# Optimization experiments

Measured on AMD Instinct MI355X. Metric: run time of the kernel, lower is better.

Reference implementation:

```python
import jax, jax.numpy as jnp
import numpy as np

PI = np.pi
WIN = (8, 8)
N = WIN[0] * WIN[1]          # 64 tokens per window
NUM_HEADS = 8
DIM = 256
HEAD_DIM = DIM // NUM_HEADS  # 32
P = 4                        # Fourier series order (hardcoded in module)
W_RES = 64                   # input_resolution[1]
SCALE = HEAD_DIM ** -0.5
B_ = 1024                    # num_windows * batch


def _azimuth():
    # relative_coords[:, :, 1] from the torch module: relative column offsets
    ch = np.arange(WIN[0])
    cw = np.arange(WIN[1])
    gh, gw = np.meshgrid(ch, cw, indexing='ij')
    cf = np.stack([gh.ravel(), gw.ravel()])          # (2, N)
    rel = cf[:, :, None] - cf[:, None, :]            # (2, N, N)
    return jnp.asarray(rel[1], dtype=jnp.float32)    # (N, N)


def setup_inputs() -> dict:
    key = jax.random.key(0)
    ks = jax.random.split(key, 12)
    std = 0.02
    return {
        'x': jax.random.normal(ks[0], (B_, N, DIM), dtype=jnp.float32),
        'D': jax.random.uniform(ks[1], (B_, N), dtype=jnp.float32),
        'a_p': std * jax.random.normal(ks[2], (P + 1, NUM_HEADS), dtype=jnp.float32),
        'b_p': std * jax.random.normal(ks[3], (P, NUM_HEADS), dtype=jnp.float32),
        'a_r': std * jax.random.normal(ks[4], (P + 1, NUM_HEADS), dtype=jnp.float32),
        'b_r': std * jax.random.normal(ks[5], (P, NUM_HEADS), dtype=jnp.float32),
        'qkv_w': std * jax.random.normal(ks[6], (3 * DIM, DIM), dtype=jnp.float32),
        'qkv_b': jnp.zeros((3 * DIM,), dtype=jnp.float32),
        'proj_w': std * jax.random.normal(ks[7], (DIM, DIM), dtype=jnp.float32),
        'proj_b': jnp.zeros((DIM,), dtype=jnp.float32),
    }


def reference(x, D, a_p, b_p, a_r, b_r, qkv_w, qkv_b, proj_w, proj_b):
    B, n, C = x.shape

    # ---- azimuth Fourier bias: A_phi, shape (H, N, N) ----
    az = _azimuth() * (2.0 * PI / W_RES)                       # (N, N)
    ii = jnp.arange(1, P + 1, dtype=x.dtype)[:, None, None]    # (P, 1, 1)
    cosP = jnp.cos(ii * az)                                    # (P, N, N)
    sinP = jnp.sin(ii * az)
    A_phi = (jnp.einsum('ph,pij->hij', a_p[1:], cosP)
             + jnp.einsum('ph,pij->hij', b_p, sinP)) / P + a_p[0][:, None, None]

    # ---- radius Fourier bias: A_r, shape (B, N, N, H); rad[b,i,j] = D[b,j] - D[b,i] ----
    rad = D[:, None, :] - D[:, :, None]                        # (B, N, N)
    r_max = 2.0                                                # module overwrites r_max = 2
    A_r = jnp.zeros(rad.shape + (NUM_HEADS,), dtype=x.dtype)
    for i in range(1, P + 1):
        arg = rad * (2.0 * PI * i / r_max)
        A_r = A_r + jnp.cos(arg)[..., None] * a_r[i] + jnp.sin(arg)[..., None] * b_r[i - 1]
    A_r = A_r / P + a_r[0]                                     # (B, N, N, H)

    # ---- attention ----
    qkv = (x @ qkv_w.T + qkv_b).reshape(B, n, 3, NUM_HEADS, HEAD_DIM)
    qkv = qkv.transpose(2, 0, 3, 1, 4)                         # (3, B, H, N, hd)
    q, k, v = qkv[0], qkv[1], qkv[2]
    attn = jnp.einsum('bhid,bhjd->bhij', q * SCALE, k)
    attn = attn + A_phi[None] + A_r.transpose(0, 3, 1, 2)
    attn = jax.nn.softmax(attn, axis=-1)
    out = jnp.einsum('bhij,bhjd->bhid', attn, v)
    out = out.transpose(0, 2, 1, 3).reshape(B, n, C)
    return out @ proj_w.T + proj_b
```

## Files before the change

kernel.cpp:

```cpp
#include <hip/hip_runtime.h>
#include <hip/hip_bf16.h>


using short8  = __attribute__((ext_vector_type(8))) short;
using short4v = __attribute__((ext_vector_type(4))) short;
using floatx4 = __attribute__((ext_vector_type(4))) float;
using uint4v  = __attribute__((ext_vector_type(4))) unsigned int;

#define PI_F    3.14159265358979323846f
#define SCALE_F 0.17677669529663687f

__device__ __forceinline__ short bfs(float x) {
  __hip_bfloat16 h = __float2bfloat16(x);
  return __builtin_bit_cast(short, h);
}

__device__ __forceinline__ unsigned pk2(float a, float b) {
  unsigned lo = (unsigned short)bfs(a);
  unsigned hi = (unsigned short)bfs(b);
  return lo | (hi << 16);
}

__global__ void prep_kernel(const float* __restrict__ qw,
                            const float* __restrict__ pw,
                            __hip_bfloat16* __restrict__ dst) {
  int g = blockIdx.x * 256 + threadIdx.x;
  const float4* src;
  __hip_bfloat16* d;
  if (g < 49152) { src = (const float4*)qw + g; d = dst + g * 4; }
  else { int g2 = g - 49152; src = (const float4*)pw + g2; d = dst + 196608 + g2 * 4; }
  float4 v = *src;
  d[0] = __float2bfloat16(v.x);
  d[1] = __float2bfloat16(v.y);
  d[2] = __float2bfloat16(v.z);
  d[3] = __float2bfloat16(v.w);
}

__device__ __forceinline__ void fourier_feats(float dv, int col, float* f) {
  float s1, c1; __sincosf(PI_F * dv, &s1, &c1);
  float c2 = c1*c1 - s1*s1, s2 = 2.f*s1*c1;
  float c3 = c2*c1 - s2*s1, s3 = s2*c1 + c2*s1;
  float c4 = c2*c2 - s2*s2, s4 = 2.f*s2*c2;
  float sa1, ca1; __sincosf((2.f * PI_F / 64.f) * (float)col, &sa1, &ca1);
  float ca2 = ca1*ca1 - sa1*sa1, sa2 = 2.f*sa1*ca1;
  float ca3 = ca2*ca1 - sa2*sa1, sa3 = sa2*ca1 + ca2*sa1;
  float ca4 = ca2*ca2 - sa2*sa2, sa4 = 2.f*sa2*ca2;
  f[0]=c1;  f[1]=c2;  f[2]=c3;  f[3]=c4;
  f[4]=s1;  f[5]=s2;  f[6]=s3;  f[7]=s4;
  f[8]=ca1; f[9]=ca2; f[10]=ca3; f[11]=ca4;
  f[12]=sa1; f[13]=sa2; f[14]=sa3; f[15]=sa4;
}

__global__ __launch_bounds__(256) void win_kernel(
    const float* __restrict__ x, const float* __restrict__ D,
    const float* __restrict__ a_p, const float* __restrict__ b_p,
    const float* __restrict__ a_r, const float* __restrict__ b_r,
    const __hip_bfloat16* __restrict__ wq, const float* __restrict__ qkv_b,
    const __hip_bfloat16* __restrict__ pwb, const float* __restrict__ pb,
    float* __restrict__ out)
{
  __shared__ __align__(16) __hip_bfloat16 sX  [64 * 256];
  __shared__ __align__(16) __hip_bfloat16 sStr[4 * 4096];
  __shared__ __align__(16) __hip_bfloat16 sQf [64 * 32];

  const int tid = threadIdx.x;
  const int lane = tid & 63, w = tid >> 6;
  const int laneN = lane & 15, laneQ = lane >> 4;
  const int b = blockIdx.x;
  const floatx4 fzero = {0.f, 0.f, 0.f, 0.f};
  const short8 zero8 = {0, 0, 0, 0, 0, 0, 0, 0};

  char* xb = (char*)sX;
  char* sb = (char*)sStr + w * 8192;

  float f[16];
  fourier_feats(D[b * 64 + lane], lane & 7, f);

  const float4* xg = (const float4*)(x + (size_t)b * 16384);
  #pragma unroll 4
  for (int it = 0; it < 16; ++it) {
    int g = tid + it * 256;
    float4 v = xg[g];
    int t = g >> 6;
    int off = (t * 512 + (g & 63) * 8) ^ ((t & 7) << 4);
    short4v pk = { bfs(v.x), bfs(v.y), bfs(v.z), bfs(v.w) };
    *(short4v*)(xb + off) = pk;
  }
  if (tid < 64) {
    int t = tid;
    uint4v q0 = { pk2(f[0],f[1]),  pk2(f[2],f[3]),  pk2(f[4],f[5]),   pk2(f[6],f[7]) };
    uint4v q1 = { pk2(f[8],f[9]),  pk2(f[10],f[11]),pk2(f[12],f[13]), pk2(f[14],f[15]) };
    uint4v zz = { 0u, 0u, 0u, 0u };
    char* qb = (char*)sQf;
    *(uint4v*)(qb + ((t * 64 +  0) ^ ((t & 3) << 4))) = q0;
    *(uint4v*)(qb + ((t * 64 + 16) ^ ((t & 3) << 4))) = q1;
    *(uint4v*)(qb + ((t * 64 + 32) ^ ((t & 3) << 4))) = zz;
    *(uint4v*)(qb + ((t * 64 + 48) ^ ((t & 3) << 4))) = zz;
  }
  __syncthreads();

  for (int hi = 0; hi < 2; ++hi) {
    const int hh = w + hi * 4;

    const __hip_bfloat16* wqQ = wq + (size_t)(      hh*32 + laneN) * 256 + laneQ * 8;
    const __hip_bfloat16* wqK = wq + (size_t)(256 + hh*32 + laneN) * 256 + laneQ * 8;
    const __hip_bfloat16* wqV = wq + (size_t)(512 + hh*32 + laneN) * 256 + laneQ * 8;

    short8 qf[4];
    {
      floatx4 Qa[4][2];
      #pragma unroll
      for (int mt = 0; mt < 4; ++mt) { Qa[mt][0]=fzero; Qa[mt][1]=fzero; }
      __builtin_amdgcn_s_setprio(1);
      #pragma unroll
      for (int kk = 0; kk < 8; ++kk) {
        short8 a4[4];
        #pragma unroll
        for (int mt = 0; mt < 4; ++mt) {
          int off = ((mt*16 + laneN) * 512 + kk*64 + laneQ*16) ^ ((laneN & 7) << 4);
          a4[mt] = *(const short8*)(xb + off);
        }
        #pragma unroll
        for (int ont = 0; ont < 2; ++ont) {
          short8 fq = *(const short8*)(wqQ + (size_t)ont*16*256 + kk*32);
          #pragma unroll
          for (int mt = 0; mt < 4; ++mt)
            Qa[mt][ont] = __builtin_amdgcn_mfma_f32_16x16x32_bf16(fq, a4[mt], Qa[mt][ont], 0, 0, 0);
        }
      }
      __builtin_amdgcn_s_setprio(0);
      float4 b0 = *(const float4*)&qkv_b[hh*32 +      laneQ*4];
      float4 b1 = *(const float4*)&qkv_b[hh*32 + 16 + laneQ*4];
      float qba[2][4] = {{b0.x,b0.y,b0.z,b0.w},{b1.x,b1.y,b1.z,b1.w}};
      #pragma unroll
      for (int mt = 0; mt < 4; ++mt)
        #pragma unroll
        for (int ont = 0; ont < 2; ++ont) {
          short4v pq;
          #pragma unroll
          for (int r = 0; r < 4; ++r)
            pq[r] = bfs((Qa[mt][ont][r] + qba[ont][r]) * SCALE_F);
          int off = ((mt*16 + laneN) * 64 + ont*32 + laneQ*8) ^ ((laneN & 3) << 4);
          *(short4v*)(sb + off) = pq;
        }
      #pragma unroll
      for (int ct = 0; ct < 4; ++ct)
        qf[ct] = *(const short8*)(sb + (((ct*16 + laneN) * 64 + laneQ*16) ^ ((laneN & 3) << 4)));
    }

    short8 kf[4];
    {
      floatx4 Ka[4][2];
      #pragma unroll
      for (int mt = 0; mt < 4; ++mt) { Ka[mt][0]=fzero; Ka[mt][1]=fzero; }
      __builtin_amdgcn_s_setprio(1);
      #pragma unroll
      for (int kk = 0; kk < 8; ++kk) {
        short8 a4[4];
        #pragma unroll
        for (int mt = 0; mt < 4; ++mt) {
          int off = ((mt*16 + laneN) * 512 + kk*64 + laneQ*16) ^ ((laneN & 7) << 4);
          a4[mt] = *(const short8*)(xb + off);
        }
        #pragma unroll
        for (int ont = 0; ont < 2; ++ont) {
          short8 fk = *(const short8*)(wqK + (size_t)ont*16*256 + kk*32);
          #pragma unroll
          for (int mt = 0; mt < 4; ++mt)
            Ka[mt][ont] = __builtin_amdgcn_mfma_f32_16x16x32_bf16(fk, a4[mt], Ka[mt][ont], 0, 0, 0);
        }
      }
      __builtin_amdgcn_s_setprio(0);
      float4 b0 = *(const float4*)&qkv_b[256 + hh*32 +      laneQ*4];
      float4 b1 = *(const float4*)&qkv_b[256 + hh*32 + 16 + laneQ*4];
      float kba[2][4] = {{b0.x,b0.y,b0.z,b0.w},{b1.x,b1.y,b1.z,b1.w}};
      #pragma unroll
      for (int mt = 0; mt < 4; ++mt)
        #pragma unroll
        for (int ont = 0; ont < 2; ++ont) {
          short4v pk;
          #pragma unroll
          for (int r = 0; r < 4; ++r)
            pk[r] = bfs(Ka[mt][ont][r] + kba[ont][r]);
          int off = ((mt*16 + laneN) * 64 + ont*32 + laneQ*8) ^ ((laneN & 3) << 4);
          *(short4v*)(sb + off) = pk;
        }
      #pragma unroll
      for (int rt = 0; rt < 4; ++rt)
        kf[rt] = *(const short8*)(sb + (((rt*16 + laneN) * 64 + laneQ*16) ^ ((laneN & 3) << 4)));
    }

    short8 kmf[4];
    {
      float m0[4], m1[4], m2[4], m3[4];
      #pragma unroll
      for (int p = 0; p < 4; ++p) {
        float ar = a_r[(p+1)*8 + hh], br = b_r[p*8 + hh];
        float ap = a_p[(p+1)*8 + hh], bp = b_p[p*8 + hh];
        m0[p] = (ar*f[p]     + br*f[4+p])  * 0.25f;
        m1[p] = (ar*f[4+p]   - br*f[p])    * 0.25f;
        m2[p] = (ap*f[8+p]   - bp*f[12+p]) * 0.25f;
        m3[p] = (ap*f[12+p]  + bp*f[8+p])  * 0.25f;
      }
      uint4v k0 = { pk2(m0[0],m0[1]), pk2(m0[2],m0[3]), pk2(m1[0],m1[1]), pk2(m1[2],m1[3]) };
      uint4v k1 = { pk2(m2[0],m2[1]), pk2(m2[2],m2[3]), pk2(m3[0],m3[1]), pk2(m3[2],m3[3]) };
      *(uint4v*)(sb + lane * 32)      = k0;
      *(uint4v*)(sb + lane * 32 + 16) = k1;
      #pragma unroll
      for (int rt = 0; rt < 4; ++rt) {
        short8 t8 = *(const short8*)(sb + (rt*16 + laneN) * 32 + (laneQ & 1) * 16);
        kmf[rt] = (laneQ < 2) ? t8 : zero8;
      }
    }
    short8 qff[4];
    #pragma unroll
    for (int ct = 0; ct < 4; ++ct)
      qff[ct] = *(const short8*)((char*)sQf + (((ct*16 + laneN) * 64 + laneQ*16) ^ ((laneN & 3) << 4)));

    short8 vf[2][2];
    {
      floatx4 Va[4][2];
      #pragma unroll
      for (int mt = 0; mt < 4; ++mt) { Va[mt][0]=fzero; Va[mt][1]=fzero; }
      __builtin_amdgcn_s_setprio(1);
      #pragma unroll
      for (int kk = 0; kk < 8; ++kk) {
        short8 a4[4];
        #pragma unroll
        for (int mt = 0; mt < 4; ++mt) {
          int off = ((mt*16 + laneN) * 512 + kk*64 + laneQ*16) ^ ((laneN & 7) << 4);
          a4[mt] = *(const short8*)(xb + off);
        }
        #pragma unroll
        for (int ont = 0; ont < 2; ++ont) {
          short8 fv = *(const short8*)(wqV + (size_t)ont*16*256 + kk*32);
          #pragma unroll
          for (int mt = 0; mt < 4; ++mt)
            Va[mt][ont] = __builtin_amdgcn_mfma_f32_16x16x32_bf16(a4[mt], fv, Va[mt][ont], 0, 0, 0);
        }
      }
      __builtin_amdgcn_s_setprio(0);
      float bv0 = qkv_b[512 + hh*32 +      laneN];
      float bv1 = qkv_b[512 + hh*32 + 16 + laneN];
      #pragma unroll
      for (int mt = 0; mt < 4; ++mt)
        #pragma unroll
        for (int ont = 0; ont < 2; ++ont) {
          float bv = ont ? bv1 : bv0;
          short4v pv;
          #pragma unroll
          for (int r = 0; r < 4; ++r)
            pv[r] = bfs(Va[mt][ont][r] + bv);
          int off = ((ont*16 + laneN) * 128 + mt*32 + laneQ*8) ^ ((laneN & 7) << 4);
          *(short4v*)(sb + off) = pv;
        }
      #pragma unroll
      for (int ont = 0; ont < 2; ++ont)
        #pragma unroll
        for (int kb = 0; kb < 2; ++kb)
          vf[ont][kb] = *(const short8*)(sb + (((ont*16 + laneN) * 128 + kb*64 + laneQ*16) ^ ((laneN & 7) << 4)));
    }

    floatx4 Oa[2][4];
    #pragma unroll
    for (int cp = 0; cp < 2; ++cp) {
      floatx4 S[4][2];
      __builtin_amdgcn_s_setprio(1);
      #pragma unroll
      for (int rt = 0; rt < 4; ++rt)
        #pragma unroll
        for (int cc = 0; cc < 2; ++cc) {
          int ct = cp * 2 + cc;
          S[rt][cc] = __builtin_amdgcn_mfma_f32_16x16x32_bf16(kf[rt], qf[ct], fzero, 0, 0, 0);
          S[rt][cc] = __builtin_amdgcn_mfma_f32_16x16x32_bf16(kmf[rt], qff[ct], S[rt][cc], 0, 0, 0);
        }
      __builtin_amdgcn_s_setprio(0);

      float inv2[2];
      #pragma unroll
      for (int cc = 0; cc < 2; ++cc) {
        float mx = S[0][cc][0];
        #pragma unroll
        for (int rt = 0; rt < 4; ++rt)
          #pragma unroll
          for (int r = 0; r < 4; ++r)
            mx = fmaxf(mx, S[rt][cc][r]);
        mx = fmaxf(mx, __shfl_xor(mx, 16));
        mx = fmaxf(mx, __shfl_xor(mx, 32));
        float sum = 0.f;
        #pragma unroll
        for (int rt = 0; rt < 4; ++rt)
          #pragma unroll
          for (int r = 0; r < 4; ++r) {
            S[rt][cc][r] = __expf(S[rt][cc][r] - mx);
            sum += S[rt][cc][r];
          }
        sum += __shfl_xor(sum, 16);
        sum += __shfl_xor(sum, 32);
        inv2[cc] = __builtin_amdgcn_rcpf(sum);
      }

      #pragma unroll
      for (int cc = 0; cc < 2; ++cc)
        #pragma unroll
        for (int rt = 0; rt < 4; ++rt) {
          short4v pp;
          #pragma unroll
          for (int r = 0; r < 4; ++r)
            pp[r] = bfs(S[rt][cc][r] * inv2[cc]);
          int off = ((cc*16 + laneN) * 128 + rt*32 + laneQ*8) ^ ((laneN & 7) << 4);
          *(short4v*)(sb + off) = pp;
        }

      __builtin_amdgcn_s_setprio(1);
      #pragma unroll
      for (int cc = 0; cc < 2; ++cc) {
        int ct = cp * 2 + cc;
        short8 pf0 = *(const short8*)(sb + (((cc*16 + laneN) * 128 +  0 + laneQ*16) ^ ((laneN & 7) << 4)));
        short8 pf1 = *(const short8*)(sb + (((cc*16 + laneN) * 128 + 64 + laneQ*16) ^ ((laneN & 7) << 4)));
        #pragma unroll
        for (int ont = 0; ont < 2; ++ont) {
          Oa[ont][ct] = __builtin_amdgcn_mfma_f32_16x16x32_bf16(vf[ont][0], pf0, fzero, 0, 0, 0);
          Oa[ont][ct] = __builtin_amdgcn_mfma_f32_16x16x32_bf16(vf[ont][1], pf1, Oa[ont][ct], 0, 0, 0);
        }
      }
      __builtin_amdgcn_s_setprio(0);
    }

    {
      int obase = hi ? 0 : 4096;
      #pragma unroll
      for (int ont = 0; ont < 2; ++ont)
        #pragma unroll
        for (int ct = 0; ct < 4; ++ct) {
          short4v po;
          #pragma unroll
          for (int r = 0; r < 4; ++r)
            po[r] = bfs(Oa[ont][ct][r]);
          int off = obase + (((ct*16 + laneN) * 64 + ont*32 + laneQ*8) ^ ((laneN & 3) << 4));
          *(short4v*)(sb + off) = po;
        }
    }
  }
  __syncthreads();

  floatx4 pacc[4][4];
  #pragma unroll
  for (int mt = 0; mt < 4; ++mt)
    #pragma unroll
    for (int n = 0; n < 4; ++n) pacc[mt][n] = fzero;

  const __hip_bfloat16* pwr = pwb + (size_t)(w*64 + laneN) * 256 + laneQ * 8;
  #pragma unroll
  for (int kk = 0; kk < 8; ++kk) {
    char* ob = (char*)sStr + (kk & 3) * 8192 + ((kk < 4) ? 4096 : 0);
    short8 pa[4];
    #pragma unroll
    for (int mt = 0; mt < 4; ++mt)
      pa[mt] = *(const short8*)(ob + (((mt*16 + laneN) * 64 + laneQ*16) ^ ((laneN & 3) << 4)));
    short8 pw4[4];
    #pragma unroll
    for (int n = 0; n < 4; ++n)
      pw4[n] = *(const short8*)(pwr + (size_t)n*16*256 + kk*32);
    __builtin_amdgcn_s_setprio(1);
    #pragma unroll
    for (int mt = 0; mt < 4; ++mt)
      #pragma unroll
      for (int n = 0; n < 4; ++n)
        pacc[mt][n] = __builtin_amdgcn_mfma_f32_16x16x32_bf16(pw4[n], pa[mt], pacc[mt][n], 0, 0, 0);
    __builtin_amdgcn_s_setprio(0);
  }

  float* og = out + (size_t)b * 16384;
  #pragma unroll
  for (int n = 0; n < 4; ++n) {
    float4 b4 = *(const float4*)&pb[w*64 + n*16 + laneQ*4];
    #pragma unroll
    for (int mt = 0; mt < 4; ++mt) {
      float4 o4;
      o4.x = pacc[mt][n][0] + b4.x;
      o4.y = pacc[mt][n][1] + b4.y;
      o4.z = pacc[mt][n][2] + b4.z;
      o4.w = pacc[mt][n][3] + b4.w;
      *(float4*)&og[(mt*16 + laneN) * 256 + w*64 + n*16 + laneQ*4] = o4;
    }
  }
}

extern "C" void kernel_launch(void* const* d_in, const int* in_sizes, int n_in,
                              void* d_out, int out_size, void* d_ws, size_t ws_size,
                              hipStream_t stream) {
  const float* x      = (const float*)d_in[0];
  const float* D      = (const float*)d_in[1];
  const float* a_p    = (const float*)d_in[2];
  const float* b_p    = (const float*)d_in[3];
  const float* a_r    = (const float*)d_in[4];
  const float* b_r    = (const float*)d_in[5];
  const float* qkv_w  = (const float*)d_in[6];
  const float* qkv_b  = (const float*)d_in[7];
  const float* proj_w = (const float*)d_in[8];
  const float* proj_b = (const float*)d_in[9];

  __hip_bfloat16* wq  = (__hip_bfloat16*)d_ws;
  __hip_bfloat16* pwb = wq + 196608;
  float* out = (float*)d_out;

  prep_kernel<<<256, 256, 0, stream>>>(qkv_w, proj_w, wq);
  win_kernel<<<1024, 256, 0, stream>>>(x, D, a_p, b_p, a_r, b_r, wq, qkv_b,
                                       pwb, proj_b, out);
}
```

Before: 244.1 us.

## Use one wave per head with 512-thread blocks and reuse x buffer for output

The block grows from 4 to 8 waves, so each wave handles a single head instead of looping over two heads, and each wave computes 32 output columns of the projection instead of 64. Per-wave scratch shrinks to 4KB, the separate Fourier-feature buffer is dropped, and the attention output is staged into the x shared buffer after a barrier. Softmax now processes one column tile at a time and keeps the output packed in registers. The aim is more parallelism per window and lower register pressure. The cost is an extra barrier and more threads competing for the same LDS and register budget under the new launch bounds.

```diff
diff --git a/kernel.cpp b/kernel.cpp
--- a/kernel.cpp
+++ b/kernel.cpp
@@ -6,6 +6,7 @@
 using short4v = __attribute__((ext_vector_type(4))) short;
 using floatx4 = __attribute__((ext_vector_type(4))) float;
 using uint4v  = __attribute__((ext_vector_type(4))) unsigned int;
+using uint2v  = __attribute__((ext_vector_type(2))) unsigned int;
 
 #define PI_F    3.14159265358979323846f
 #define SCALE_F 0.17677669529663687f
@@ -51,7 +52,7 @@
   f[12]=sa1; f[13]=sa2; f[14]=sa3; f[15]=sa4;
 }
 
-__global__ __launch_bounds__(256) void win_kernel(
+__global__ __launch_bounds__(512, 4) void win_kernel(
     const float* __restrict__ x, const float* __restrict__ D,
     const float* __restrict__ a_p, const float* __restrict__ b_p,
     const float* __restrict__ a_r, const float* __restrict__ b_r,
@@ -60,8 +61,7 @@
     float* __restrict__ out)
 {
   __shared__ __align__(16) __hip_bfloat16 sX  [64 * 256];
-  __shared__ __align__(16) __hip_bfloat16 sStr[4 * 4096];
-  __shared__ __align__(16) __hip_bfloat16 sQf [64 * 32];
+  __shared__ __align__(16) __hip_bfloat16 sStr[8 * 2048];
 
   const int tid = threadIdx.x;
   const int lane = tid & 63, w = tid >> 6;
@@ -71,310 +71,288 @@
   const short8 zero8 = {0, 0, 0, 0, 0, 0, 0, 0};
 
   char* xb = (char*)sX;
-  char* sb = (char*)sStr + w * 8192;
-
-  float f[16];
-  fourier_feats(D[b * 64 + lane], lane & 7, f);
-
+  char* sb = (char*)sStr + w * 4096;
+
+  {
+    float f[16];
+    fourier_feats(D[b * 64 + lane], lane & 7, f);
+    uint4v q0 = { pk2(f[0],f[1]),  pk2(f[2],f[3]),  pk2(f[4],f[5]),   pk2(f[6],f[7]) };
+    uint4v q1 = { pk2(f[8],f[9]),  pk2(f[10],f[11]),pk2(f[12],f[13]), pk2(f[14],f[15]) };
+    uint4v zz = { 0u, 0u, 0u, 0u };
+    *(uint4v*)(sb + ((lane * 64 +  0) ^ ((lane & 3) << 4))) = q0;
+    *(uint4v*)(sb + ((lane * 64 + 16) ^ ((lane & 3) << 4))) = q1;
+    *(uint4v*)(sb + ((lane * 64 + 32) ^ ((lane & 3) << 4))) = zz;
+    *(uint4v*)(sb + ((lane * 64 + 48) ^ ((lane & 3) << 4))) = zz;
+  }
   const float4* xg = (const float4*)(x + (size_t)b * 16384);
-  #pragma unroll 4
-  for (int it = 0; it < 16; ++it) {
-    int g = tid + it * 256;
+  #pragma unroll
+  for (int it = 0; it < 8; ++it) {
+    int g = tid + it * 512;
     float4 v = xg[g];
     int t = g >> 6;
     int off = (t * 512 + (g & 63) * 8) ^ ((t & 7) << 4);
     short4v pk = { bfs(v.x), bfs(v.y), bfs(v.z), bfs(v.w) };
     *(short4v*)(xb + off) = pk;
   }
-  if (tid < 64) {
-    int t = tid;
-    uint4v q0 = { pk2(f[0],f[1]),  pk2(f[2],f[3]),  pk2(f[4],f[5]),   pk2(f[6],f[7]) };
-    uint4v q1 = { pk2(f[8],f[9]),  pk2(f[10],f[11]),pk2(f[12],f[13]), pk2(f[14],f[15]) };
-    uint4v zz = { 0u, 0u, 0u, 0u };
-    char* qb = (char*)sQf;
-    *(uint4v*)(qb + ((t * 64 +  0) ^ ((t & 3) << 4))) = q0;
-    *(uint4v*)(qb + ((t * 64 + 16) ^ ((t & 3) << 4))) = q1;
-    *(uint4v*)(qb + ((t * 64 + 32) ^ ((t & 3) << 4))) = zz;
-    *(uint4v*)(qb + ((t * 64 + 48) ^ ((t & 3) << 4))) = zz;
-  }
+  short8 qff[4];
+  #pragma unroll
+  for (int ct = 0; ct < 4; ++ct)
+    qff[ct] = *(const short8*)(sb + (((ct*16 + laneN) * 64 + laneQ*16) ^ ((laneN & 3) << 4)));
   __syncthreads();
 
-  for (int hi = 0; hi < 2; ++hi) {
-    const int hh = w + hi * 4;
-
-    const __hip_bfloat16* wqQ = wq + (size_t)(      hh*32 + laneN) * 256 + laneQ * 8;
-    const __hip_bfloat16* wqK = wq + (size_t)(256 + hh*32 + laneN) * 256 + laneQ * 8;
-    const __hip_bfloat16* wqV = wq + (size_t)(512 + hh*32 + laneN) * 256 + laneQ * 8;
-
-    short8 qf[4];
-    {
-      floatx4 Qa[4][2];
-      #pragma unroll
-      for (int mt = 0; mt < 4; ++mt) { Qa[mt][0]=fzero; Qa[mt][1]=fzero; }
-      __builtin_amdgcn_s_setprio(1);
-      #pragma unroll
-      for (int kk = 0; kk < 8; ++kk) {
-        short8 a4[4];
-        #pragma unroll
-        for (int mt = 0; mt < 4; ++mt) {
-          int off = ((mt*16 + laneN) * 512 + kk*64 + laneQ*16) ^ ((laneN & 7) << 4);
-          a4[mt] = *(const short8*)(xb + off);
-        }
-        #pragma unroll
-        for (int ont = 0; ont < 2; ++ont) {
-          short8 fq = *(const short8*)(wqQ + (size_t)ont*16*256 + kk*32);
-          #pragma unroll
-          for (int mt = 0; mt < 4; ++mt)
-            Qa[mt][ont] = __builtin_amdgcn_mfma_f32_16x16x32_bf16(fq, a4[mt], Qa[mt][ont], 0, 0, 0);
-        }
-      }
-      __builtin_amdgcn_s_setprio(0);
-      float4 b0 = *(const float4*)&qkv_b[hh*32 +      laneQ*4];
-      float4 b1 = *(const float4*)&qkv_b[hh*32 + 16 + laneQ*4];
-      float qba[2][4] = {{b0.x,b0.y,b0.z,b0.w},{b1.x,b1.y,b1.z,b1.w}};
-      #pragma unroll
-      for (int mt = 0; mt < 4; ++mt)
-        #pragma unroll
-        for (int ont = 0; ont < 2; ++ont) {
-          short4v pq;
-          #pragma unroll
-          for (int r = 0; r < 4; ++r)
-            pq[r] = bfs((Qa[mt][ont][r] + qba[ont][r]) * SCALE_F);
-          int off = ((mt*16 + laneN) * 64 + ont*32 + laneQ*8) ^ ((laneN & 3) << 4);
-          *(short4v*)(sb + off) = pq;
-        }
-      #pragma unroll
-      for (int ct = 0; ct < 4; ++ct)
-        qf[ct] = *(const short8*)(sb + (((ct*16 + laneN) * 64 + laneQ*16) ^ ((laneN & 3) << 4)));
-    }
-
-    short8 kf[4];
-    {
-      floatx4 Ka[4][2];
-      #pragma unroll
-      for (int mt = 0; mt < 4; ++mt) { Ka[mt][0]=fzero; Ka[mt][1]=fzero; }
-      __builtin_amdgcn_s_setprio(1);
-      #pragma unroll
-      for (int kk = 0; kk < 8; ++kk) {
-        short8 a4[4];
-        #pragma unroll
-        for (int mt = 0; mt < 4; ++mt) {
-          int off = ((mt*16 + laneN) * 512 + kk*64 + laneQ*16) ^ ((laneN & 7) << 4);
-          a4[mt] = *(const short8*)(xb + off);
-        }
-        #pragma unroll
-        for (int ont = 0; ont < 2; ++ont) {
-          short8 fk = *(const short8*)(wqK + (size_t)ont*16*256 + kk*32);
-          #pragma unroll
-          for (int mt = 0; mt < 4; ++mt)
-            Ka[mt][ont] = __builtin_amdgcn_mfma_f32_16x16x32_bf16(fk, a4[mt], Ka[mt][ont], 0, 0, 0);
-        }
-      }
-      __builtin_amdgcn_s_setprio(0);
-      float4 b0 = *(const float4*)&qkv_b[256 + hh*32 +      laneQ*4];
-      float4 b1 = *(const float4*)&qkv_b[256 + hh*32 + 16 + laneQ*4];
-      float kba[2][4] = {{b0.x,b0.y,b0.z,b0.w},{b1.x,b1.y,b1.z,b1.w}};
-      #pragma unroll
-      for (int mt = 0; mt < 4; ++mt)
-        #pragma unroll
-        for (int ont = 0; ont < 2; ++ont) {
-          short4v pk;
-          #pragma unroll
-          for (int r = 0; r < 4; ++r)
-            pk[r] = bfs(Ka[mt][ont][r] + kba[ont][r]);
-          int off = ((mt*16 + laneN) * 64 + ont*32 + laneQ*8) ^ ((laneN & 3) << 4);
-          *(short4v*)(sb + off) = pk;
-        }
-      #pragma unroll
-      for (int rt = 0; rt < 4; ++rt)
-        kf[rt] = *(const short8*)(sb + (((rt*16 + laneN) * 64 + laneQ*16) ^ ((laneN & 3) << 4)));
-    }
-
-    short8 kmf[4];
-    {
-      float m0[4], m1[4], m2[4], m3[4];
-      #pragma unroll
-      for (int p = 0; p < 4; ++p) {
-        float ar = a_r[(p+1)*8 + hh], br = b_r[p*8 + hh];
-        float ap = a_p[(p+1)*8 + hh], bp = b_p[p*8 + hh];
-        m0[p] = (ar*f[p]     + br*f[4+p])  * 0.25f;
-        m1[p] = (ar*f[4+p]   - br*f[p])    * 0.25f;
-        m2[p] = (ap*f[8+p]   - bp*f[12+p]) * 0.25f;
-        m3[p] = (ap*f[12+p]  + bp*f[8+p])  * 0.25f;
-      }
-      uint4v k0 = { pk2(m0[0],m0[1]), pk2(m0[2],m0[3]), pk2(m1[0],m1[1]), pk2(m1[2],m1[3]) };
-      uint4v k1 = { pk2(m2[0],m2[1]), pk2(m2[2],m2[3]), pk2(m3[0],m3[1]), pk2(m3[2],m3[3]) };
-      *(uint4v*)(sb + lane * 32)      = k0;
-      *(uint4v*)(sb + lane * 32 + 16) = k1;
-      #pragma unroll
-      for (int rt = 0; rt < 4; ++rt) {
-        short8 t8 = *(const short8*)(sb + (rt*16 + laneN) * 32 + (laneQ & 1) * 16);
-        kmf[rt] = (laneQ < 2) ? t8 : zero8;
-      }
-    }
-    short8 qff[4];
+  const int hh = w;
+  const __hip_bfloat16* wqQ = wq + (size_t)(      hh*32 + laneN) * 256 + laneQ * 8;
+  const __hip_bfloat16* wqK = wq + (size_t)(256 + hh*32 + laneN) * 256 + laneQ * 8;
+  const __hip_bfloat16* wqV = wq + (size_t)(512 + hh*32 + laneN) * 256 + laneQ * 8;
+
+  short8 qf[4];
+  {
+    floatx4 Qa[4][2];
+    #pragma unroll
+    for (int mt = 0; mt < 4; ++mt) { Qa[mt][0]=fzero; Qa[mt][1]=fzero; }
+    __builtin_amdgcn_s_setprio(1);
+    #pragma unroll
+    for (int kk = 0; kk < 8; ++kk) {
+      short8 a4[4];
+      #pragma unroll
+      for (int mt = 0; mt < 4; ++mt) {
+        int off = ((mt*16 + laneN) * 512 + kk*64 + laneQ*16) ^ ((laneN & 7) << 4);
+        a4[mt] = *(const short8*)(xb + off);
+      }
+      #pragma unroll
+      for (int ont = 0; ont < 2; ++ont) {
+        short8 fq = *(const short8*)(wqQ + (size_t)ont*16*256 + kk*32);
+        #pragma unroll
+        for (int mt = 0; mt < 4; ++mt)
+          Qa[mt][ont] = __builtin_amdgcn_mfma_f32_16x16x32_bf16(fq, a4[mt], Qa[mt][ont], 0, 0, 0);
+      }
+    }
+    __builtin_amdgcn_s_setprio(0);
+    float4 b0 = *(const float4*)&qkv_b[hh*32 +      laneQ*4];
+    float4 b1 = *(const float4*)&qkv_b[hh*32 + 16 + laneQ*4];
+    float qba[2][4] = {{b0.x,b0.y,b0.z,b0.w},{b1.x,b1.y,b1.z,b1.w}};
+    #pragma unroll
+    for (int mt = 0; mt < 4; ++mt)
+      #pragma unroll
+      for (int ont = 0; ont < 2; ++ont) {
+        short4v pq;
+        #pragma unroll
+        for (int r = 0; r < 4; ++r)
+          pq[r] = bfs((Qa[mt][ont][r] + qba[ont][r]) * SCALE_F);
+        int off = ((mt*16 + laneN) * 64 + ont*32 + laneQ*8) ^ ((laneN & 3) << 4);
+        *(short4v*)(sb + off) = pq;
+      }
     #pragma unroll
     for (int ct = 0; ct < 4; ++ct)
-      qff[ct] = *(const short8*)((char*)sQf + (((ct*16 + laneN) * 64 + laneQ*16) ^ ((laneN & 3) << 4)));
-
-    short8 vf[2][2];
-    {
-      floatx4 Va[4][2];
-      #pragma unroll
-      for (int mt = 0; mt < 4; ++mt) { Va[mt][0]=fzero; Va[mt][1]=fzero; }
-      __builtin_amdgcn_s_setprio(1);
-      #pragma unroll
-      for (int kk = 0; kk < 8; ++kk) {
-        short8 a4[4];
-        #pragma unroll
-        for (int mt = 0; mt < 4; ++mt) {
-          int off = ((mt*16 + laneN) * 512 + kk*64 + laneQ*16) ^ ((laneN & 7) << 4);
-          a4[mt] = *(const short8*)(xb + off);
-        }
-        #pragma unroll
-        for (int ont = 0; ont < 2; ++ont) {
-          short8 fv = *(const short8*)(wqV + (size_t)ont*16*256 + kk*32);
-          #pragma unroll
-          for (int mt = 0; mt < 4; ++mt)
-            Va[mt][ont] = __builtin_amdgcn_mfma_f32_16x16x32_bf16(a4[mt], fv, Va[mt][ont], 0, 0, 0);
-        }
-      }
-      __builtin_amdgcn_s_setprio(0);
-      float bv0 = qkv_b[512 + hh*32 +      laneN];
-      float bv1 = qkv_b[512 + hh*32 + 16 + laneN];
-      #pragma unroll
-      for (int mt = 0; mt < 4; ++mt)
-        #pragma unroll
-        for (int ont = 0; ont < 2; ++ont) {
-          float bv = ont ? bv1 : bv0;
-          short4v pv;
-          #pragma unroll
-          for (int r = 0; r < 4; ++r)
-            pv[r] = bfs(Va[mt][ont][r] + bv);
-          int off = ((ont*16 + laneN) * 128 + mt*32 + laneQ*8) ^ ((laneN & 7) << 4);
-          *(short4v*)(sb + off) = pv;
-        }
-      #pragma unroll
-      for (int ont = 0; ont < 2; ++ont)
-        #pragma unroll
-        for (int kb = 0; kb < 2; ++kb)
-          vf[ont][kb] = *(const short8*)(sb + (((ont*16 + laneN) * 128 + kb*64 + laneQ*16) ^ ((laneN & 7) << 4)));
-    }
-
-    floatx4 Oa[2][4];
-    #pragma unroll
-    for (int cp = 0; cp < 2; ++cp) {
-      floatx4 S[4][2];
-      __builtin_amdgcn_s_setprio(1);
-      #pragma unroll
-      for (int rt = 0; rt < 4; ++rt)
-        #pragma unroll
-        for (int cc = 0; cc < 2; ++cc) {
-          int ct = cp * 2 + cc;
-          S[rt][cc] = __builtin_amdgcn_mfma_f32_16x16x32_bf16(kf[rt], qf[ct], fzero, 0, 0, 0);
-          S[rt][cc] = __builtin_amdgcn_mfma_f32_16x16x32_bf16(kmf[rt], qff[ct], S[rt][cc], 0, 0, 0);
-        }
-      __builtin_amdgcn_s_setprio(0);
-
-      float inv2[2];
-      #pragma unroll
-      for (int cc = 0; cc < 2; ++cc) {
-        float mx = S[0][cc][0];
-        #pragma unroll
-        for (int rt = 0; rt < 4; ++rt)
-          #pragma unroll
-          for (int r = 0; r < 4; ++r)
-            mx = fmaxf(mx, S[rt][cc][r]);
-        mx = fmaxf(mx, __shfl_xor(mx, 16));
-        mx = fmaxf(mx, __shfl_xor(mx, 32));
-        float sum = 0.f;
-        #pragma unroll
-        for (int rt = 0; rt < 4; ++rt)
-          #pragma unroll
-          for (int r = 0; r < 4; ++r) {
-            S[rt][cc][r] = __expf(S[rt][cc][r] - mx);
-            sum += S[rt][cc][r];
-          }
-        sum += __shfl_xor(sum, 16);
-        sum += __shfl_xor(sum, 32);
-        inv2[cc] = __builtin_amdgcn_rcpf(sum);
-      }
-
-      #pragma unroll
-      for (int cc = 0; cc < 2; ++cc)
-        #pragma unroll
-        for (int rt = 0; rt < 4; ++rt) {
-          short4v pp;
-          #pragma unroll
-          for (int r = 0; r < 4; ++r)
-            pp[r] = bfs(S[rt][cc][r] * inv2[cc]);
-          int off = ((cc*16 + laneN) * 128 + rt*32 + laneQ*8) ^ ((laneN & 7) << 4);
-          *(short4v*)(sb + off) = pp;
-        }
-
-      __builtin_amdgcn_s_setprio(1);
-      #pragma unroll
-      for (int cc = 0; cc < 2; ++cc) {
-        int ct = cp * 2 + cc;
-        short8 pf0 = *(const short8*)(sb + (((cc*16 + laneN) * 128 +  0 + laneQ*16) ^ ((laneN & 7) << 4)));
-        short8 pf1 = *(const short8*)(sb + (((cc*16 + laneN) * 128 + 64 + laneQ*16) ^ ((laneN & 7) << 4)));
-        #pragma unroll
-        for (int ont = 0; ont < 2; ++ont) {
-          Oa[ont][ct] = __builtin_amdgcn_mfma_f32_16x16x32_bf16(vf[ont][0], pf0, fzero, 0, 0, 0);
-          Oa[ont][ct] = __builtin_amdgcn_mfma_f32_16x16x32_bf16(vf[ont][1], pf1, Oa[ont][ct], 0, 0, 0);
-        }
-      }
-      __builtin_amdgcn_s_setprio(0);
-    }
-
-    {
-      int obase = hi ? 0 : 4096;
-      #pragma unroll
-      for (int ont = 0; ont < 2; ++ont)
-        #pragma unroll
-        for (int ct = 0; ct < 4; ++ct) {
-          short4v po;
-          #pragma unroll
-          for (int r = 0; r < 4; ++r)
-            po[r] = bfs(Oa[ont][ct][r]);
-          int off = obase + (((ct*16 + laneN) * 64 + ont*32 + laneQ*8) ^ ((laneN & 3) << 4));
-          *(short4v*)(sb + off) = po;
-        }
-    }
-  }
+      qf[ct] = *(const short8*)(sb + (((ct*16 + laneN) * 64 + laneQ*16) ^ ((laneN & 3) << 4)));
+  }
+
+  short8 kf[4];
+  {
+    floatx4 Ka[4][2];
+    #pragma unroll
+    for (int mt = 0; mt < 4; ++mt) { Ka[mt][0]=fzero; Ka[mt][1]=fzero; }
+    __builtin_amdgcn_s_setprio(1);
+    #pragma unroll
+    for (int kk = 0; kk < 8; ++kk) {
+      short8 a4[4];
+      #pragma unroll
+      for (int mt = 0; mt < 4; ++mt) {
+        int off = ((mt*16 + laneN) * 512 + kk*64 + laneQ*16) ^ ((laneN & 7) << 4);
+        a4[mt] = *(const short8*)(xb + off);
+      }
+      #pragma unroll
+      for (int ont = 0; ont < 2; ++ont) {
+        short8 fk = *(const short8*)(wqK + (size_t)ont*16*256 + kk*32);
+        #pragma unroll
+        for (int mt = 0; mt < 4; ++mt)
+          Ka[mt][ont] = __builtin_amdgcn_mfma_f32_16x16x32_bf16(fk, a4[mt], Ka[mt][ont], 0, 0, 0);
+      }
+    }
+    __builtin_amdgcn_s_setprio(0);
+    float4 b0 = *(const float4*)&qkv_b[256 + hh*32 +      laneQ*4];
+    float4 b1 = *(const float4*)&qkv_b[256 + hh*32 + 16 + laneQ*4];
+    float kba[2][4] = {{b0.x,b0.y,b0.z,b0.w},{b1.x,b1.y,b1.z,b1.w}};
+    #pragma unroll
+    for (int mt = 0; mt < 4; ++mt)
+      #pragma unroll
+      for (int ont = 0; ont < 2; ++ont) {
+        short4v pk;
+        #pragma unroll
+        for (int r = 0; r < 4; ++r)
+          pk[r] = bfs(Ka[mt][ont][r] + kba[ont][r]);
+        int off = ((mt*16 + laneN) * 64 + ont*32 + laneQ*8) ^ ((laneN & 3) << 4);
+        *(short4v*)(sb + off) = pk;
+      }
+    #pragma unroll
+    for (int rt = 0; rt < 4; ++rt)
+      kf[rt] = *(const short8*)(sb + (((rt*16 + laneN) * 64 + laneQ*16) ^ ((laneN & 3) << 4)));
+  }
+
+  short8 kmf[4];
+  {
+    float f[16];
+    fourier_feats(D[b * 64 + lane], lane & 7, f);
+    float m0[4], m1[4], m2[4], m3[4];
+    #pragma unroll
+    for (int p = 0; p < 4; ++p) {
+      float ar = a_r[(p+1)*8 + hh], br = b_r[p*8 + hh];
+      float ap = a_p[(p+1)*8 + hh], bp = b_p[p*8 + hh];
+      m0[p] = (ar*f[p]     + br*f[4+p])  * 0.25f;
+      m1[p] = (ar*f[4+p]   - br*f[p])    * 0.25f;
+      m2[p] = (ap*f[8+p]   - bp*f[12+p]) * 0.25f;
+      m3[p] = (ap*f[12+p]  + bp*f[8+p])  * 0.25f;
+    }
+    uint4v k0 = { pk2(m0[0],m0[1]), pk2(m0[2],m0[3]), pk2(m1[0],m1[1]), pk2(m1[2],m1[3]) };
+    uint4v k1 = { pk2(m2[0],m2[1]), pk2(m2[2],m2[3]), pk2(m3[0],m3[1]), pk2(m3[2],m3[3]) };
+    *(uint4v*)(sb + lane * 32)      = k0;
+    *(uint4v*)(sb + lane * 32 + 16) = k1;
+    #pragma unroll
+    for (int rt = 0; rt < 4; ++rt) {
+      short8 t8 = *(const short8*)(sb + (rt*16 + laneN) * 32 + (laneQ & 1) * 16);
+      kmf[rt] = (laneQ < 2) ? t8 : zero8;
+    }
+  }
+
+  short8 vf[2][2];
+  {
+    floatx4 Va[4][2];
+    #pragma unroll
+    for (int mt = 0; mt < 4; ++mt) { Va[mt][0]=fzero; Va[mt][1]=fzero; }
+    __builtin_amdgcn_s_setprio(1);
+    #pragma unroll
+    for (int kk = 0; kk < 8; ++kk) {
+      short8 a4[4];
+      #pragma unroll
+      for (int mt = 0; mt < 4; ++mt) {
+        int off = ((mt*16 + laneN) * 512 + kk*64 + laneQ*16) ^ ((laneN & 7) << 4);
+        a4[mt] = *(const short8*)(xb + off);
+      }
+      #pragma unroll
+      for (int ont = 0; ont < 2; ++ont) {
+        short8 fv = *(const short8*)(wqV + (size_t)ont*16*256 + kk*32);
+        #pragma unroll
+        for (int mt = 0; mt < 4; ++mt)
+          Va[mt][ont] = __builtin_amdgcn_mfma_f32_16x16x32_bf16(a4[mt], fv, Va[mt][ont], 0, 0, 0);
+      }
+    }
+    __builtin_amdgcn_s_setprio(0);
+    float bv0 = qkv_b[512 + hh*32 +      laneN];
+    float bv1 = qkv_b[512 + hh*32 + 16 + laneN];
+    #pragma unroll
+    for (int mt = 0; mt < 4; ++mt)
+      #pragma unroll
+      for (int ont = 0; ont < 2; ++ont) {
+        float bv = ont ? bv1 : bv0;
+        short4v pv;
+        #pragma unroll
+        for (int r = 0; r < 4; ++r)
+          pv[r] = bfs(Va[mt][ont][r] + bv);
+        int off = ((ont*16 + laneN) * 128 + mt*32 + laneQ*8) ^ ((laneN & 7) << 4);
+        *(short4v*)(sb + off) = pv;
+      }
+    #pragma unroll
+    for (int ont = 0; ont < 2; ++ont)
+      #pragma unroll
+      for (int kb = 0; kb < 2; ++kb)
+        vf[ont][kb] = *(const short8*)(sb + (((ont*16 + laneN) * 128 + kb*64 + laneQ*16) ^ ((laneN & 7) << 4)));
+  }
+
+  unsigned opk[2][4][2];
+  #pragma unroll
+  for (int ct = 0; ct < 4; ++ct) {
+    floatx4 S[4];
+    __builtin_amdgcn_s_setprio(1);
+    #pragma unroll
+    for (int rt = 0; rt < 4; ++rt) {
+      S[rt] = __builtin_amdgcn_mfma_f32_16x16x32_bf16(kf[rt], qf[ct], fzero, 0, 0, 0);
+      S[rt] = __builtin_amdgcn_mfma_f32_16x16x32_bf16(kmf[rt], qff[ct], S[rt], 0, 0, 0);
+    }
+    __builtin_amdgcn_s_setprio(0);
+
+    float mx = S[0][0];
+    #pragma unroll
+    for (int rt = 0; rt < 4; ++rt)
+      #pragma unroll
+      for (int r = 0; r < 4; ++r)
+        mx = fmaxf(mx, S[rt][r]);
+    mx = fmaxf(mx, __shfl_xor(mx, 16));
+    mx = fmaxf(mx, __shfl_xor(mx, 32));
+    float sum = 0.f;
+    #pragma unroll
+    for (int rt = 0; rt < 4; ++rt)
+      #pragma unroll
+      for (int r = 0; r < 4; ++r) {
+        S[rt][r] = __expf(S[rt][r] - mx);
+        sum += S[rt][r];
+      }
+    sum += __shfl_xor(sum, 16);
+    sum += __shfl_xor(sum, 32);
+    float inv = __builtin_amdgcn_rcpf(sum);
+
+    #pragma unroll
+    for (int rt = 0; rt < 4; ++rt) {
+      short4v pp;
+      #pragma unroll
+      for (int r = 0; r < 4; ++r)
+        pp[r] = bfs(S[rt][r] * inv);
+      int off = (laneN * 128 + rt*32 + laneQ*8) ^ ((laneN & 7) << 4);
+      *(short4v*)(sb + off) = pp;
+    }
+    short8 pf0 = *(const short8*)(sb + ((laneN * 128 +      laneQ*16) ^ ((laneN & 7) << 4)));
+    short8 pf1 = *(const short8*)(sb + ((laneN * 128 + 64 + laneQ*16) ^ ((laneN & 7) << 4)));
+    __builtin_amdgcn_s_setprio(1);
+    floatx4 O0 = __builtin_amdgcn_mfma_f32_16x16x32_bf16(vf[0][0], pf0, fzero, 0, 0, 0);
+    O0 = __builtin_amdgcn_mfma_f32_16x16x32_bf16(vf[0][1], pf1, O0, 0, 0, 0);
+    floatx4 O1 = __builtin_amdgcn_mfma_f32_16x16x32_bf16(vf[1][0], pf0, fzero, 0, 0, 0);
+    O1 = __builtin_amdgcn_mfma_f32_16x16x32_bf16(vf[1][1], pf1, O1, 0, 0, 0);
+    __builtin_amdgcn_s_setprio(0);
+    opk[0][ct][0] = pk2(O0[0], O0[1]);
+    opk[0][ct][1] = pk2(O0[2], O0[3]);
+    opk[1][ct][0] = pk2(O1[0], O1[1]);
+    opk[1][ct][1] = pk2(O1[2], O1[3]);
+  }
+
   __syncthreads();
-
-  floatx4 pacc[4][4];
-  #pragma unroll
-  for (int mt = 0; mt < 4; ++mt)
-    #pragma unroll
-    for (int n = 0; n < 4; ++n) pacc[mt][n] = fzero;
-
-  const __hip_bfloat16* pwr = pwb + (size_t)(w*64 + laneN) * 256 + laneQ * 8;
+  #pragma unroll
+  for (int ont = 0; ont < 2; ++ont)
+    #pragma unroll
+    for (int ct = 0; ct < 4; ++ct) {
+      uint2v po = { opk[ont][ct][0], opk[ont][ct][1] };
+      int off = w * 4096 + (((ct*16 + laneN) * 64 + ont*32 + laneQ*8) ^ ((laneN & 3) << 4));
+      *(uint2v*)(xb + off) = po;
+    }
+  __syncthreads();
+
+  floatx4 pacc[4][2];
+  #pragma unroll
+  for (int mt = 0; mt < 4; ++mt) { pacc[mt][0] = fzero; pacc[mt][1] = fzero; }
+  const __hip_bfloat16* pwr = pwb + (size_t)(w*32 + laneN) * 256 + laneQ * 8;
   #pragma unroll
   for (int kk = 0; kk < 8; ++kk) {
-    char* ob = (char*)sStr + (kk & 3) * 8192 + ((kk < 4) ? 4096 : 0);
+    char* ob = xb + kk * 4096;
     short8 pa[4];
     #pragma unroll
     for (int mt = 0; mt < 4; ++mt)
       pa[mt] = *(const short8*)(ob + (((mt*16 + laneN) * 64 + laneQ*16) ^ ((laneN & 3) << 4)));
-    short8 pw4[4];
-    #pragma unroll
-    for (int n = 0; n < 4; ++n)
+    short8 pw4[2];
+    #pragma unroll
+    for (int n = 0; n < 2; ++n)
       pw4[n] = *(const short8*)(pwr + (size_t)n*16*256 + kk*32);
     __builtin_amdgcn_s_setprio(1);
     #pragma unroll
     for (int mt = 0; mt < 4; ++mt)
       #pragma unroll
-      for (int n = 0; n < 4; ++n)
+      for (int n = 0; n < 2; ++n)
         pacc[mt][n] = __builtin_amdgcn_mfma_f32_16x16x32_bf16(pw4[n], pa[mt], pacc[mt][n], 0, 0, 0);
     __builtin_amdgcn_s_setprio(0);
   }
 
   float* og = out + (size_t)b * 16384;
   #pragma unroll
-  for (int n = 0; n < 4; ++n) {
-    float4 b4 = *(const float4*)&pb[w*64 + n*16 + laneQ*4];
+  for (int n = 0; n < 2; ++n) {
+    int col0 = w * 32 + n * 16;
+    float4 b4 = *(const float4*)&pb[col0 + laneQ * 4];
     #pragma unroll
     for (int mt = 0; mt < 4; ++mt) {
       float4 o4;
@@ -382,7 +360,7 @@
       o4.y = pacc[mt][n][1] + b4.y;
       o4.z = pacc[mt][n][2] + b4.z;
       o4.w = pacc[mt][n][3] + b4.w;
-      *(float4*)&og[(mt*16 + laneN) * 256 + w*64 + n*16 + laneQ*4] = o4;
+      *(float4*)&og[(mt*16 + laneN) * 256 + col0 + laneQ*4] = o4;
     }
   }
 }
@@ -406,6 +384,6 @@
   float* out = (float*)d_out;
 
   prep_kernel<<<256, 256, 0, stream>>>(qkv_w, proj_w, wq);
-  win_kernel<<<1024, 256, 0, stream>>>(x, D, a_p, b_p, a_r, b_r, wq, qkv_b,
+  win_kernel<<<1024, 512, 0, stream>>>(x, D, a_p, b_p, a_r, b_r, wq, qkv_b,
                                        pwb, proj_b, out);
 }
```

After: 231.3 us. -5.2%, faster.
